# Kernel optimization log

Measured on AMD Instinct MI355X. Metric: run time of the kernel, lower is better.

## Reference

```python
import jax, jax.numpy as jnp
import numpy as np

USER = 50000
ITEM = 50000
N = USER + ITEM          # total nodes
D = 64                   # latdim
H = 128                  # hyperNum
E = 1600000              # number of nonzeros in sparse adj
LAYERS = 2               # gnn_layer
LEAKY = 0.5              # negative_slope


def setup_inputs() -> dict:
    key = jax.random.key(0)
    ks = jax.random.split(key, 7)
    adj_rows = jax.random.randint(ks[0], (E,), 0, N, dtype=jnp.int32)
    adj_cols = jax.random.randint(ks[1], (E,), 0, N, dtype=jnp.int32)
    adj_vals = jax.random.uniform(ks[2], (E,), dtype=jnp.float32)
    uEmbeds = jax.random.normal(ks[3], (USER, D), dtype=jnp.float32) * 0.02
    iEmbeds = jax.random.normal(ks[4], (ITEM, D), dtype=jnp.float32) * 0.02
    Hyper = jax.random.normal(ks[5], (D, H), dtype=jnp.float32) * 0.02
    zishiying = jax.random.normal(ks[6], (N, D), dtype=jnp.float32) * 0.02
    return {"adj_rows": adj_rows, "adj_cols": adj_cols, "adj_vals": adj_vals,
            "uEmbeds": uEmbeds, "iEmbeds": iEmbeds, "Hyper": Hyper,
            "zishiying": zishiying, "keepRate": 1}


def _leaky(x):
    return jax.nn.leaky_relu(x, negative_slope=LEAKY)


def _spmm(rows, cols, vals, x):
    # out[r, :] = sum_{e: rows[e]==r} vals[e] * x[cols[e], :]
    return jax.ops.segment_sum(vals[:, None] * x[cols], rows, num_segments=N)


def reference(adj_rows, adj_cols, adj_vals, uEmbeds, iEmbeds, Hyper, zishiying, keepRate):
    kr = float(keepRate)
    embeds0 = jnp.concatenate([uEmbeds, iEmbeds], axis=0)  # [N, D]
    allHyper = embeds0 @ Hyper                              # [N, H]
    aij = jax.nn.sigmoid(zishiying) * 2.0 - 1.0             # [N, D]
    cur = embeds0
    hyperLats = []
    tem = embeds0
    key = jax.random.key(42)
    for _ in range(LAYERS):
        vals = adj_vals
        hyp = allHyper
        if kr < 1.0:  # static python branch: edge drop + dropout
            key, k1, k2 = jax.random.split(key, 3)
            emask = jnp.floor(jax.random.uniform(k1, (E,)) + kr)
            vals = adj_vals * emask / kr
            dmask = (jax.random.uniform(k2, allHyper.shape) < kr).astype(allHyper.dtype)
            hyp = allHyper * dmask / kr
        # GCN: sigmoid-gated sparse propagation
        tem = _leaky(_spmm(adj_rows, adj_cols, vals, cur * aij))  # [N, D]
        # HGNN: dense hypergraph two-hop propagation
        lat = _leaky(hyp.T @ cur)                                  # [H, D]
        hyperLat = _leaky(hyp @ lat)                               # [N, D]
        hyperLats.append(hyperLat)
        cur = hyperLat + tem
    # stack final embeds (temEmbeds) with the per-layer hyper lats
    return jnp.stack([tem] + hyperLats, axis=0)  # [LAYERS+1, N, D]
```

## Files before the change

kernel.cpp:

```cpp
#include <hip/hip_runtime.h>
#include <hip/hip_bf16.h>

typedef unsigned short u16;

#define NN    100000
#define NU    50000
#define DD    64
#define HHY   128
#define EE    1600000
#define NCHK  384
#define CROWS 261
#define NSB   391
#define SCB   6250
#define LPB   768
#define BUCKW 400000

__device__ __forceinline__ float us2f(u16 u) {
    union { unsigned int i; float f; } v; v.i = ((unsigned int)u) << 16; return v.f;
}
__device__ __forceinline__ u16 f2us(float f) {
    __hip_bfloat16 b = __float2bfloat16(f);
    return *reinterpret_cast<u16*>(&b);
}
__device__ __forceinline__ float lrelu(float x) { return x > 0.f ? x : 0.5f * x; }


__device__ __forceinline__ void allhyper_body(int ab, float* hlds,
        const float4* __restrict__ u, const float4* __restrict__ it,
        const float* __restrict__ Hyper, u16* __restrict__ hyp) {
    int t = threadIdx.x;
    const float4* hsrc = (const float4*)Hyper;
    float4* hdst = (float4*)hlds;
#pragma unroll
    for (int i = 0; i < 8; i++) hdst[i * 256 + t] = hsrc[i * 256 + t];
    __syncthreads();
    int hg = t & 31;
    int rs = t >> 5;
    int n0 = ab * 16 + rs * 2;
    int n1 = n0 + 1;
    const float4* s0 = (n0 < NU) ? (u + (size_t)n0 * 16) : (it + (size_t)(n0 - NU) * 16);
    const float4* s1 = (n1 < NU) ? (u + (size_t)n1 * 16) : (it + (size_t)(n1 - NU) * 16);
    float a00 = 0.f, a01 = 0.f, a02 = 0.f, a03 = 0.f;
    float a10 = 0.f, a11 = 0.f, a12 = 0.f, a13 = 0.f;
#pragma unroll
    for (int half = 0; half < 2; half++) {
        float4 e0[8], e1[8];
#pragma unroll
        for (int i = 0; i < 8; i++) { e0[i] = s0[half * 8 + i]; e1[i] = s1[half * 8 + i]; }
#pragma unroll
        for (int i = 0; i < 8; i++) {
            float ev0[4] = { e0[i].x, e0[i].y, e0[i].z, e0[i].w };
            float ev1[4] = { e1[i].x, e1[i].y, e1[i].z, e1[i].w };
#pragma unroll
            for (int k = 0; k < 4; k++) {
                int d = half * 32 + i * 4 + k;
                float4 hq = *(const float4*)(hlds + d * HHY + hg * 4);
                a00 += ev0[k] * hq.x; a01 += ev0[k] * hq.y;
                a02 += ev0[k] * hq.z; a03 += ev0[k] * hq.w;
                a10 += ev1[k] * hq.x; a11 += ev1[k] * hq.y;
                a12 += ev1[k] * hq.z; a13 += ev1[k] * hq.w;
            }
        }
    }
    u16* o0 = hyp + (size_t)n0 * HHY + hg * 4;
    o0[0] = f2us(a00); o0[1] = f2us(a01); o0[2] = f2us(a02); o0[3] = f2us(a03);
    u16* o1 = hyp + (size_t)n1 * HHY + hg * 4;
    o1[0] = f2us(a10); o1[1] = f2us(a11); o1[2] = f2us(a12); o1[3] = f2us(a13);
}

__device__ __forceinline__ void latpart_body(int chunk, int yy,
        const u16* __restrict__ cur, const u16* __restrict__ hyp,
        float* __restrict__ part) {
    int t = threadIdx.x;
    int w = t >> 6, d = t & 63;
    int h0 = (yy * 4 + w) * 16;
    int c0 = chunk * CROWS;
    int c1 = c0 + CROWS; if (c1 > NN) c1 = NN;
    float acc[16];
#pragma unroll
    for (int j = 0; j < 16; j++) acc[j] = 0.f;
    int n = c0;
    for (; n + 4 <= c1; n += 4) {
        const u16* cp = cur + (size_t)n * DD + d;
        u16 ca = cp[0], cb = cp[DD], cc = cp[2 * DD], cd = cp[3 * DD];
        const ushort4* ha4 = (const ushort4*)(hyp + (size_t)n * HHY + h0);
        const ushort4* hb4 = (const ushort4*)(hyp + (size_t)(n + 1) * HHY + h0);
        const ushort4* hc4 = (const ushort4*)(hyp + (size_t)(n + 2) * HHY + h0);
        const ushort4* hd4 = (const ushort4*)(hyp + (size_t)(n + 3) * HHY + h0);
        u16 ua[16], ub[16], uc[16], ud[16];
        *(ushort4*)(ua + 0) = ha4[0]; *(ushort4*)(ua + 4) = ha4[1];
        *(ushort4*)(ua + 8) = ha4[2]; *(ushort4*)(ua + 12) = ha4[3];
        *(ushort4*)(ub + 0) = hb4[0]; *(ushort4*)(ub + 4) = hb4[1];
        *(ushort4*)(ub + 8) = hb4[2]; *(ushort4*)(ub + 12) = hb4[3];
        *(ushort4*)(uc + 0) = hc4[0]; *(ushort4*)(uc + 4) = hc4[1];
        *(ushort4*)(uc + 8) = hc4[2]; *(ushort4*)(uc + 12) = hc4[3];
        *(ushort4*)(ud + 0) = hd4[0]; *(ushort4*)(ud + 4) = hd4[1];
        *(ushort4*)(ud + 8) = hd4[2]; *(ushort4*)(ud + 12) = hd4[3];
        float fa = us2f(ca), fb = us2f(cb), fc = us2f(cc), fd = us2f(cd);
#pragma unroll
        for (int j = 0; j < 16; j++)
            acc[j] += us2f(ua[j]) * fa + us2f(ub[j]) * fb
                    + us2f(uc[j]) * fc + us2f(ud[j]) * fd;
    }
    for (; n < c1; n++) {
        float cv = us2f(cur[(size_t)n * DD + d]);
        const ushort4* hp = (const ushort4*)(hyp + (size_t)n * HHY + h0);
        u16 ha[16];
        *(ushort4*)(ha + 0)  = hp[0];
        *(ushort4*)(ha + 4)  = hp[1];
        *(ushort4*)(ha + 8)  = hp[2];
        *(ushort4*)(ha + 12) = hp[3];
#pragma unroll
        for (int j = 0; j < 16; j++) acc[j] += us2f(ha[j]) * cv;
    }
#pragma unroll
    for (int j = 0; j < 16; j++)
        part[((size_t)chunk * HHY + h0 + j) * DD + d] = acc[j];
}

__device__ __forceinline__ void scatter_body(int chunk, int bucket,
        const int* __restrict__ pos,
        const int* __restrict__ cols, const float* __restrict__ vals,
        int2* __restrict__ csr) {
    int e = chunk * 256 + threadIdx.x;
    int p = pos[e];
    if ((unsigned)p / (unsigned)BUCKW == (unsigned)bucket) {
        csr[p] = make_int2(cols[e], __float_as_int(vals[e]));
    }
}

__device__ __forceinline__ void spmm_body(int b,
        const int* __restrict__ row_start, const int2* __restrict__ csr,
        const u16* __restrict__ gate, float* __restrict__ out0) {
    int w = threadIdx.x >> 6, d = threadIdx.x & 63;
    int row = b * 4 + w;
    int s = row_start[row], e = row_start[row + 1];
    float a0 = 0.f, a1 = 0.f, a2 = 0.f, a3 = 0.f;
    float a4 = 0.f, a5 = 0.f, a6 = 0.f, a7 = 0.f;
    int j = s;
    for (; j + 8 <= e; j += 8) {
        int2 c0 = csr[j],     c1 = csr[j + 1], c2 = csr[j + 2], c3 = csr[j + 3];
        int2 c4 = csr[j + 4], c5 = csr[j + 5], c6 = csr[j + 6], c7 = csr[j + 7];
        float g0 = us2f(gate[(size_t)c0.x * DD + d]);
        float g1 = us2f(gate[(size_t)c1.x * DD + d]);
        float g2 = us2f(gate[(size_t)c2.x * DD + d]);
        float g3 = us2f(gate[(size_t)c3.x * DD + d]);
        float g4 = us2f(gate[(size_t)c4.x * DD + d]);
        float g5 = us2f(gate[(size_t)c5.x * DD + d]);
        float g6 = us2f(gate[(size_t)c6.x * DD + d]);
        float g7 = us2f(gate[(size_t)c7.x * DD + d]);
        a0 += __int_as_float(c0.y) * g0;
        a1 += __int_as_float(c1.y) * g1;
        a2 += __int_as_float(c2.y) * g2;
        a3 += __int_as_float(c3.y) * g3;
        a4 += __int_as_float(c4.y) * g4;
        a5 += __int_as_float(c5.y) * g5;
        a6 += __int_as_float(c6.y) * g6;
        a7 += __int_as_float(c7.y) * g7;
    }
    for (; j + 4 <= e; j += 4) {
        int2 c0 = csr[j], c1 = csr[j + 1], c2 = csr[j + 2], c3 = csr[j + 3];
        float g0 = us2f(gate[(size_t)c0.x * DD + d]);
        float g1 = us2f(gate[(size_t)c1.x * DD + d]);
        float g2 = us2f(gate[(size_t)c2.x * DD + d]);
        float g3 = us2f(gate[(size_t)c3.x * DD + d]);
        a0 += __int_as_float(c0.y) * g0;
        a1 += __int_as_float(c1.y) * g1;
        a2 += __int_as_float(c2.y) * g2;
        a3 += __int_as_float(c3.y) * g3;
    }
    for (; j < e; j++) {
        int2 cv = csr[j];
        a0 += __int_as_float(cv.y) * us2f(gate[(size_t)cv.x * DD + d]);
    }
    float acc = ((a0 + a1) + (a2 + a3)) + ((a4 + a5) + (a6 + a7));
    out0[(size_t)row * DD + d] = lrelu(acc);
}

__device__ __forceinline__ void latreduce_body(int lb,
        const float* __restrict__ part, float* __restrict__ lat) {
    int idx = lb * 256 + threadIdx.x;
    float s0 = 0.f, s1 = 0.f, s2 = 0.f, s3 = 0.f;
    for (int c = 0; c < NCHK; c += 4) {
        s0 += part[(size_t)(c + 0) * HHY * DD + idx];
        s1 += part[(size_t)(c + 1) * HHY * DD + idx];
        s2 += part[(size_t)(c + 2) * HHY * DD + idx];
        s3 += part[(size_t)(c + 3) * HHY * DD + idx];
    }
    lat[idx] = lrelu((s0 + s1) + (s2 + s3));
}


__global__ __launch_bounds__(256) void k_hp_ah(const int* __restrict__ rows,
                                               int* __restrict__ cnt,
                                               int* __restrict__ ranks,
                                               const float4* __restrict__ u,
                                               const float4* __restrict__ it,
                                               ushort4* __restrict__ cur,
                                               const float* __restrict__ Hyper,
                                               u16* __restrict__ hyp,
                                               const float4* __restrict__ z,
                                               ushort4* __restrict__ gate0) {
    __shared__ float hlds[DD * HHY];
    int bid = blockIdx.x;
    int p = bid & 1, q = bid >> 1;
    if (p == 0) {
        int e = q * 256 + threadIdx.x;
        const int HALF = NU * DD / 4;
        float4 f = (e < HALF) ? u[e] : it[e - HALF];
        ushort4 c; c.x = f2us(f.x); c.y = f2us(f.y); c.z = f2us(f.z); c.w = f2us(f.w);
        cur[e] = c;
        float4 zz = z[e];
        ushort4 g;
        g.x = f2us(us2f(c.x) * (2.f / (1.f + __expf(-zz.x)) - 1.f));
        g.y = f2us(us2f(c.y) * (2.f / (1.f + __expf(-zz.y)) - 1.f));
        g.z = f2us(us2f(c.z) * (2.f / (1.f + __expf(-zz.z)) - 1.f));
        g.w = f2us(us2f(c.w) * (2.f / (1.f + __expf(-zz.w)) - 1.f));
        gate0[e] = g;
        ranks[e] = atomicAdd(&cnt[rows[e]], 1);
    } else {
        allhyper_body(q, hlds, u, it, Hyper, hyp);
    }
}

__global__ __launch_bounds__(256) void k_blocksum(const int* __restrict__ cnt,
                                                  int* __restrict__ bsum) {
    __shared__ int s[256];
    int t = threadIdx.x;
    int i = blockIdx.x * 256 + t;
    s[t] = (i < NN) ? cnt[i] : 0;
    __syncthreads();
    for (int off = 128; off > 0; off >>= 1) {
        if (t < off) s[t] += s[t + off];
        __syncthreads();
    }
    if (t == 0) bsum[blockIdx.x] = s[0];
}

__global__ __launch_bounds__(512) void k_scanb(int* __restrict__ bsum) {
    __shared__ int s[512];
    int t = threadIdx.x;
    int v = (t < NSB) ? bsum[t] : 0;
    s[t] = v;
    __syncthreads();
    for (int off = 1; off < 512; off <<= 1) {
        int add = (t >= off) ? s[t - off] : 0;
        __syncthreads();
        s[t] += add;
        __syncthreads();
    }
    if (t < NSB) bsum[t] = s[t] - v;
}

__global__ __launch_bounds__(256) void k_scanfinal(const int* __restrict__ cnt,
                                                   const int* __restrict__ bsum,
                                                   int* __restrict__ row_start) {
    __shared__ int s[256];
    int t = threadIdx.x;
    int i = blockIdx.x * 256 + t;
    int v = (i < NN) ? cnt[i] : 0;
    s[t] = v;
    __syncthreads();
    for (int off = 1; off < 256; off <<= 1) {
        int add = (t >= off) ? s[t - off] : 0;
        __syncthreads();
        s[t] += add;
        __syncthreads();
    }
    int excl = s[t] - v + bsum[blockIdx.x];
    if (i < NN) row_start[i] = excl;
    if (i == NN - 1) row_start[NN] = excl + v;
}

__global__ __launch_bounds__(256) void k_pos(const int* __restrict__ rows,
                                             const int* __restrict__ ranks,
                                             const int* __restrict__ row_start,
                                             int* __restrict__ pos) {
    int e = blockIdx.x * 256 + threadIdx.x;
    pos[e] = row_start[rows[e]] + ranks[e];
}

__global__ __launch_bounds__(256) void k_fused0(const int* __restrict__ pos,
                                                const int* __restrict__ cols,
                                                const float* __restrict__ vals,
                                                int2* __restrict__ csr,
                                                const u16* __restrict__ cur,
                                                const u16* __restrict__ hyp,
                                                float* __restrict__ part) {
    int bid = blockIdx.x;
    if (bid < LPB) {
        latpart_body(bid >> 1, bid & 1, cur, hyp, part);
    } else {
        int sid = bid - LPB;
        int xcd = sid & 7;
        int bucket = xcd & 3;
        int chunk = (sid >> 3) * 2 + (xcd >> 2);
        scatter_body(chunk, bucket, pos, cols, vals, csr);
    }
}

__global__ __launch_bounds__(256) void k_fused_sl(const int* __restrict__ row_start,
                                                  const int2* __restrict__ csr,
                                                  const u16* __restrict__ gate,
                                                  float* __restrict__ out0,
                                                  const float* __restrict__ part,
                                                  float* __restrict__ lat) {
    int bid = blockIdx.x;
    if (bid < 32) latreduce_body(bid, part, lat);
    else          spmm_body(bid - 32, row_start, csr, gate, out0);
}

__global__ __launch_bounds__(256) void k_latpart1(const u16* __restrict__ cur,
                                                  const u16* __restrict__ hyp,
                                                  float* __restrict__ part) {
    int bid = blockIdx.x;
    latpart_body(bid >> 1, bid & 1, cur, hyp, part);
}

__global__ __launch_bounds__(256) void k_hyperlat(const u16* __restrict__ hyp,
                                                  const float* __restrict__ lat,
                                                  const float* __restrict__ tem0,
                                                  float* __restrict__ outL,
                                                  u16* __restrict__ cur,
                                                  const float* __restrict__ z,
                                                  u16* __restrict__ gate,
                                                  int emit) {
    __shared__ float lds[HHY * DD];
    int t = threadIdx.x;
    for (int i = t; i < HHY * DD / 4; i += 256)
        ((float4*)lds)[i] = ((const float4*)lat)[i];
    __syncthreads();
    int w = t >> 6, l = t & 63;
    int rl = l >> 2, dq = l & 3;
    int r = blockIdx.x * 16 + rl;
    int d0 = w * 16 + dq * 4;
    float a0 = 0.f, a1 = 0.f, a2 = 0.f, a3 = 0.f;
    const u16* hrow = hyp + (size_t)r * HHY;
    for (int h0 = 0; h0 < HHY; h0 += 8) {
        ushort4 p0 = *(const ushort4*)(hrow + h0);
        ushort4 p1 = *(const ushort4*)(hrow + h0 + 4);
        u16 hv[8] = { p0.x, p0.y, p0.z, p0.w, p1.x, p1.y, p1.z, p1.w };
#pragma unroll
        for (int j = 0; j < 8; j++) {
            float hvf = us2f(hv[j]);
            float4 lv = *(const float4*)(lds + (h0 + j) * DD + d0);
            a0 += hvf * lv.x; a1 += hvf * lv.y;
            a2 += hvf * lv.z; a3 += hvf * lv.w;
        }
    }
    size_t off = (size_t)r * DD + d0;
    float h0_ = lrelu(a0), h1_ = lrelu(a1), h2_ = lrelu(a2), h3_ = lrelu(a3);
    float4 tem = *(const float4*)(tem0 + off);
    *(float4*)(outL + off) = make_float4(h0_, h1_, h2_, h3_);
    ushort4 cb;
    cb.x = f2us(h0_ + tem.x); cb.y = f2us(h1_ + tem.y);
    cb.z = f2us(h2_ + tem.z); cb.w = f2us(h3_ + tem.w);
    *(ushort4*)(cur + off) = cb;
    if (emit) {
        float4 zz = *(const float4*)(z + off);
        ushort4 g;
        g.x = f2us(us2f(cb.x) * (2.f / (1.f + __expf(-zz.x)) - 1.f));
        g.y = f2us(us2f(cb.y) * (2.f / (1.f + __expf(-zz.y)) - 1.f));
        g.z = f2us(us2f(cb.z) * (2.f / (1.f + __expf(-zz.z)) - 1.f));
        g.w = f2us(us2f(cb.w) * (2.f / (1.f + __expf(-zz.w)) - 1.f));
        *(ushort4*)(gate + off) = g;
    }
}


extern "C" void kernel_launch(void* const* d_in, const int* in_sizes, int n_in,
                              void* d_out, int out_size, void* d_ws, size_t ws_size,
                              hipStream_t stream) {
    const int*   rows  = (const int*)d_in[0];
    const int*   cols  = (const int*)d_in[1];
    const float* vals  = (const float*)d_in[2];
    const float* uEmb  = (const float*)d_in[3];
    const float* iEmb  = (const float*)d_in[4];
    const float* Hyper = (const float*)d_in[5];
    const float* zishi = (const float*)d_in[6];

    float* out = (float*)d_out;

    char* ws = (char*)d_ws;
    int2*  csr       = (int2*)(ws + 0);
    int*   row_start = (int*)(ws + 12800000);
    int*   counts    = (int*)(ws + 13600128);
    u16*   hyp       = (u16*)(ws + 14000128);
    u16*   cur       = (u16*)(ws + 39600128);
    float* lat       = (float*)(ws + 52400128);
    int*   bsum      = (int*)(ws + 52432896);

    char*  slab2 = (char*)(out + (size_t)2 * NN * DD);
    u16*   gate0 = (u16*)(out + (size_t)1 * NN * DD);
    int*   ranks = (int*)slab2;
    int*   pos   = (int*)(slab2 + 6400000);
    u16*   gate1 = (u16*)slab2;
    float* part  = (float*)(slab2 + 12800000);

    hipMemsetAsync(counts, 0, NN * sizeof(int), stream);
    k_hp_ah<<<2 * SCB, 256, 0, stream>>>(rows, counts, ranks,
                                         (const float4*)uEmb, (const float4*)iEmb,
                                         (ushort4*)cur, Hyper, hyp,
                                         (const float4*)zishi, (ushort4*)gate0);
    k_blocksum<<<NSB, 256, 0, stream>>>(counts, bsum);
    k_scanb<<<1, 512, 0, stream>>>(bsum);
    k_scanfinal<<<NSB, 256, 0, stream>>>(counts, bsum, row_start);
    k_pos<<<SCB, 256, 0, stream>>>(rows, ranks, row_start, pos);

    float* out0 = out;

    k_fused0<<<LPB + 8 * 3125, 256, 0, stream>>>(pos, cols, vals, csr, cur, hyp, part);
    k_fused_sl<<<NN / 4 + 32, 256, 0, stream>>>(row_start, csr, gate0, out0, part, lat);
    k_hyperlat<<<NN / 16, 256, 0, stream>>>(hyp, lat, out0, out + (size_t)1 * NN * DD, cur,
                                            zishi, gate1, 1);

    k_latpart1<<<LPB, 256, 0, stream>>>(cur, hyp, part);
    k_fused_sl<<<NN / 4 + 32, 256, 0, stream>>>(row_start, csr, gate1, out0, part, lat);
    k_hyperlat<<<NN / 16, 256, 0, stream>>>(hyp, lat, out0, out + (size_t)2 * NN * DD, cur,
                                            zishi, gate1, 0);
}
```

Before: 527.3 us.

## Compute hyp^T·cur partial products with bf16 MFMA via LDS staging

Replaces the scalar FMA loop that computes per-chunk partial sums of hyp^T @ cur with MFMA 16x16x32 bf16 instructions. Each block stages 32-row tiles of cur and its half of hyp into padded shared memory, then builds MFMA operands from LDS. Chunk size changes so the 100000 rows divide into 32-row tiles (352 chunks of 288 rows). It adds two barriers per tile and strided scalar LDS reads when building operands, which may limit throughput.

```diff
diff --git a/kernel.cpp b/kernel.cpp
--- a/kernel.cpp
+++ b/kernel.cpp
@@ -2,17 +2,19 @@
 #include <hip/hip_bf16.h>
 
 typedef unsigned short u16;
+typedef short bf16x8 __attribute__((ext_vector_type(8)));
+typedef float f32x4 __attribute__((ext_vector_type(4)));
 
 #define NN    100000
 #define NU    50000
 #define DD    64
 #define HHY   128
 #define EE    1600000
-#define NCHK  384
-#define CROWS 261
+#define NCHK  352
+#define CROWS 288
 #define NSB   391
 #define SCB   6250
-#define LPB   768
+#define LPB   704
 #define BUCKW 400000
 
 __device__ __forceinline__ float us2f(u16 u) {
@@ -68,54 +70,54 @@
     o1[0] = f2us(a10); o1[1] = f2us(a11); o1[2] = f2us(a12); o1[3] = f2us(a13);
 }
 
-__device__ __forceinline__ void latpart_body(int chunk, int yy,
-        const u16* __restrict__ cur, const u16* __restrict__ hyp,
-        float* __restrict__ part) {
-    int t = threadIdx.x;
-    int w = t >> 6, d = t & 63;
-    int h0 = (yy * 4 + w) * 16;
+__device__ __forceinline__ void latpart_mfma(int chunk, int half,
+        const u16* __restrict__ cur_g, const u16* __restrict__ hyp_g,
+        float* __restrict__ part, u16* sc, u16* sh) {
+    int t = threadIdx.x;
+    int w = t >> 6, l = t & 63;
+    int r = l & 15, kb = l >> 4;
+    int hbase = half * 64;
     int c0 = chunk * CROWS;
     int c1 = c0 + CROWS; if (c1 > NN) c1 = NN;
-    float acc[16];
-#pragma unroll
-    for (int j = 0; j < 16; j++) acc[j] = 0.f;
-    int n = c0;
-    for (; n + 4 <= c1; n += 4) {
-        const u16* cp = cur + (size_t)n * DD + d;
-        u16 ca = cp[0], cb = cp[DD], cc = cp[2 * DD], cd = cp[3 * DD];
-        const ushort4* ha4 = (const ushort4*)(hyp + (size_t)n * HHY + h0);
-        const ushort4* hb4 = (const ushort4*)(hyp + (size_t)(n + 1) * HHY + h0);
-        const ushort4* hc4 = (const ushort4*)(hyp + (size_t)(n + 2) * HHY + h0);
-        const ushort4* hd4 = (const ushort4*)(hyp + (size_t)(n + 3) * HHY + h0);
-        u16 ua[16], ub[16], uc[16], ud[16];
-        *(ushort4*)(ua + 0) = ha4[0]; *(ushort4*)(ua + 4) = ha4[1];
-        *(ushort4*)(ua + 8) = ha4[2]; *(ushort4*)(ua + 12) = ha4[3];
-        *(ushort4*)(ub + 0) = hb4[0]; *(ushort4*)(ub + 4) = hb4[1];
-        *(ushort4*)(ub + 8) = hb4[2]; *(ushort4*)(ub + 12) = hb4[3];
-        *(ushort4*)(uc + 0) = hc4[0]; *(ushort4*)(uc + 4) = hc4[1];
-        *(ushort4*)(uc + 8) = hc4[2]; *(ushort4*)(uc + 12) = hc4[3];
-        *(ushort4*)(ud + 0) = hd4[0]; *(ushort4*)(ud + 4) = hd4[1];
-        *(ushort4*)(ud + 8) = hd4[2]; *(ushort4*)(ud + 12) = hd4[3];
-        float fa = us2f(ca), fb = us2f(cb), fc = us2f(cc), fd = us2f(cd);
-#pragma unroll
-        for (int j = 0; j < 16; j++)
-            acc[j] += us2f(ua[j]) * fa + us2f(ub[j]) * fb
-                    + us2f(uc[j]) * fc + us2f(ud[j]) * fd;
-    }
-    for (; n < c1; n++) {
-        float cv = us2f(cur[(size_t)n * DD + d]);
-        const ushort4* hp = (const ushort4*)(hyp + (size_t)n * HHY + h0);
-        u16 ha[16];
-        *(ushort4*)(ha + 0)  = hp[0];
-        *(ushort4*)(ha + 4)  = hp[1];
-        *(ushort4*)(ha + 8)  = hp[2];
-        *(ushort4*)(ha + 12) = hp[3];
-#pragma unroll
-        for (int j = 0; j < 16; j++) acc[j] += us2f(ha[j]) * cv;
-    }
-#pragma unroll
-    for (int j = 0; j < 16; j++)
-        part[((size_t)chunk * HHY + h0 + j) * DD + d] = acc[j];
+    f32x4 acc0 = {0.f, 0.f, 0.f, 0.f};
+    f32x4 acc1 = acc0, acc2 = acc0, acc3 = acc0;
+    int srow = t >> 3, scol = (t & 7) * 8;
+    for (int n0 = c0; n0 < c1; n0 += 32) {
+        const u16* cg = cur_g + (size_t)(n0 + srow) * DD + scol;
+        const u16* hg = hyp_g + (size_t)(n0 + srow) * HHY + hbase + scol;
+        *(ushort4*)(sc + srow * 68 + scol)     = *(const ushort4*)(cg);
+        *(ushort4*)(sc + srow * 68 + scol + 4) = *(const ushort4*)(cg + 4);
+        *(ushort4*)(sh + srow * 68 + scol)     = *(const ushort4*)(hg);
+        *(ushort4*)(sh + srow * 68 + scol + 4) = *(const ushort4*)(hg + 4);
+        __syncthreads();
+        bf16x8 a;
+#pragma unroll
+        for (int j = 0; j < 8; j++)
+            a[j] = (short)sh[(kb * 8 + j) * 68 + w * 16 + r];
+        bf16x8 b0, b1, b2, b3;
+#pragma unroll
+        for (int j = 0; j < 8; j++) {
+            int ro = (kb * 8 + j) * 68 + r;
+            b0[j] = (short)sc[ro];
+            b1[j] = (short)sc[ro + 16];
+            b2[j] = (short)sc[ro + 32];
+            b3[j] = (short)sc[ro + 48];
+        }
+        acc0 = __builtin_amdgcn_mfma_f32_16x16x32_bf16(a, b0, acc0, 0, 0, 0);
+        acc1 = __builtin_amdgcn_mfma_f32_16x16x32_bf16(a, b1, acc1, 0, 0, 0);
+        acc2 = __builtin_amdgcn_mfma_f32_16x16x32_bf16(a, b2, acc2, 0, 0, 0);
+        acc3 = __builtin_amdgcn_mfma_f32_16x16x32_bf16(a, b3, acc3, 0, 0, 0);
+        __syncthreads();
+    }
+    size_t base = ((size_t)chunk * HHY + hbase + w * 16 + kb * 4) * DD + r;
+#pragma unroll
+    for (int q = 0; q < 4; q++) {
+        float* p = part + base + (size_t)q * DD;
+        p[0]  = acc0[q];
+        p[16] = acc1[q];
+        p[32] = acc2[q];
+        p[48] = acc3[q];
+    }
 }
 
 __device__ __forceinline__ void scatter_body(int chunk, int bucket,
@@ -287,9 +289,11 @@
                                                 const u16* __restrict__ cur,
                                                 const u16* __restrict__ hyp,
                                                 float* __restrict__ part) {
+    __shared__ u16 sc[32 * 68];
+    __shared__ u16 sh[32 * 68];
     int bid = blockIdx.x;
     if (bid < LPB) {
-        latpart_body(bid >> 1, bid & 1, cur, hyp, part);
+        latpart_mfma(bid >> 1, bid & 1, cur, hyp, part, sc, sh);
     } else {
         int sid = bid - LPB;
         int xcd = sid & 7;
@@ -313,8 +317,10 @@
 __global__ __launch_bounds__(256) void k_latpart1(const u16* __restrict__ cur,
                                                   const u16* __restrict__ hyp,
                                                   float* __restrict__ part) {
+    __shared__ u16 sc[32 * 68];
+    __shared__ u16 sh[32 * 68];
     int bid = blockIdx.x;
-    latpart_body(bid >> 1, bid & 1, cur, hyp, part);
+    latpart_mfma(bid >> 1, bid & 1, cur, hyp, part, sc, sh);
 }
 
 __global__ __launch_bounds__(256) void k_hyperlat(const u16* __restrict__ hyp,
```

Result: faster. 445.8 us (-15.4%).
